# Optimization experiments

Measured on AMD Instinct MI355X. Metric: run time of the kernel, lower is better.

Reference implementation:

```python
import jax, jax.numpy as jnp
import numpy as np

M_CH = 3        # channel index from shapelet_info['pos'][1]
DIL = 4         # dilation
EPS = 1e-8      # pDic['scale_epsilon']


def setup_inputs() -> dict:
    key = jax.random.key(0)
    k1, k2 = jax.random.split(key, 2)
    B, C, Q, L = 512, 8, 4096, 32
    W = Q - (L - 1) * DIL  # 3972
    x = jax.random.normal(k1, (B, C, Q), dtype=jnp.float32)
    shapelet = jax.random.normal(k2, (L,), dtype=jnp.float32)
    posMap = jnp.zeros((W,), dtype=jnp.float32)
    posSlope = jnp.float32(1.0)
    return {"x": x, "shapelet": shapelet, "posMap": posMap, "posSlope": posSlope, "ep": 1}


def reference(x, shapelet, posMap, posSlope, ep):
    # x: [B, C, Q]; pick channel m, dilated unfold -> [B, W, L]
    B, C, Q = x.shape
    L = shapelet.shape[0]
    W = Q - (L - 1) * DIL
    xc = x[:, M_CH, :]                                        # [B, Q]
    idx = jnp.arange(W)[:, None] + jnp.arange(L)[None, :] * DIL  # [W, L]
    xu = xc[:, idx]                                           # [B, W, L]
    # scaleType == 2: z-normalize each subsequence (torch.std is unbiased -> ddof=1)
    mean = jnp.mean(xu, axis=-1, keepdims=True)
    std = jnp.std(xu, axis=-1, ddof=1, keepdims=True)
    xu = (xu - mean) / (std + EPS)
    # squared distance, mean over L
    d = jnp.mean((shapelet[None, None, :] - xu) ** 2, axis=-1)  # [B, W]
    # positional weighting: posSlope*elu(-posMap) + 2.0
    w = posSlope * jax.nn.elu(-posMap) + 2.0                  # [W]
    ftrs = d * w[None, :]                                     # [B, W] (sum over singleton channel dim is identity)
    agg = jnp.min(ftrs, axis=-1)                              # [B]
    return jax.nn.relu(agg)[:, None]                          # [B, 1]
```

## Files before the change

kernel.cpp:

```cpp
#include <hip/hip_runtime.h>
#include <math.h>

#define LC  32
#define QC  4096
#define WC  3972
#define NU  993
#define RUN 8

__device__ __forceinline__ int skew(int a) { return a + (a >> 6); }

__global__ __launch_bounds__(512, 4) void feature_kernel(
    const float* __restrict__ x,
    const float* __restrict__ shp,
    const float* __restrict__ posMap,
    const float* __restrict__ posSlope_p,
    float* __restrict__ out,
    int C)
{
    __shared__ float sx[4352];
    __shared__ float sw[4160];
    __shared__ float smin[8];

    const int tid   = threadIdx.x;
    const int b     = blockIdx.x;
    const float* __restrict__ xr = x + ((size_t)b * C + 3) * QC;

    {
        const float4* xr4 = reinterpret_cast<const float4*>(xr);
        #pragma unroll
        for (int i = 0; i < 2; ++i) {
            int a4 = tid + i * 512;
            float4 v = xr4[a4];
            int s = skew(a4 * 4);
            sx[s] = v.x; sx[s+1] = v.y; sx[s+2] = v.z; sx[s+3] = v.w;
        }
    }
    {
        const float ps = posSlope_p[0];
        const float4* pm4 = reinterpret_cast<const float4*>(posMap);
        #pragma unroll
        for (int i = 0; i < 2; ++i) {
            int a4 = tid + i * 512;
            if (a4 < NU) {
                float4 z = pm4[a4];
                float e0 = (-z.x > 0.f) ? -z.x : (__expf(-z.x) - 1.f);
                float e1 = (-z.y > 0.f) ? -z.y : (__expf(-z.y) - 1.f);
                float e2 = (-z.z > 0.f) ? -z.z : (__expf(-z.z) - 1.f);
                float e3 = (-z.w > 0.f) ? -z.w : (__expf(-z.w) - 1.f);
                int s = skew(a4 * 4);
                sw[s]   = fmaf(ps, e0, 2.0f);
                sw[s+1] = fmaf(ps, e1, 2.0f);
                sw[s+2] = fmaf(ps, e2, 2.0f);
                sw[s+3] = fmaf(ps, e3, 2.0f);
            }
        }
    }

    float sreg[LC];
    #pragma unroll
    for (int j = 0; j < LC; ++j) sreg[j] = shp[j];
    float Ssum = 0.f, S2 = 0.f;
    #pragma unroll
    for (int j = 0; j < LC; ++j) { Ssum += sreg[j]; S2 = fmaf(sreg[j], sreg[j], S2); }
    const float C0 = S2 * (1.0f / 32.0f) + 31.0f / 32.0f;

    __syncthreads();

    const int lane  = tid & 63;
    const int wv_id = tid >> 6;
    const int r     = wv_id & 3;
    const int gl    = ((wv_id >> 2) << 6) | lane;
    const int u0    = gl * RUN;
    const int w0    = r + 4 * u0;

    float buf[32];
    #pragma unroll
    for (int p = 0; p < 32; ++p)
        buf[p] = sx[skew(w0 + 4 * p)];

    float a0=0,a1=0,a2=0,a3=0, q0=0,q1=0,q2=0,q3=0;
    #pragma unroll
    for (int p = 0; p < 32; p += 4) {
        a0 += buf[p];   q0 = fmaf(buf[p],   buf[p],   q0);
        a1 += buf[p+1]; q1 = fmaf(buf[p+1], buf[p+1], q1);
        a2 += buf[p+2]; q2 = fmaf(buf[p+2], buf[p+2], q2);
        a3 += buf[p+3]; q3 = fmaf(buf[p+3], buf[p+3], q3);
    }
    float sum = (a0+a1)+(a2+a3);
    float sq  = (q0+q1)+(q2+q3);

    float best = INFINITY;

    #pragma unroll
    for (int k = 0; k < RUN; ++k) {
        if (k > 0) {
            int slot = (k + 31) & 31;
            float oldv = buf[slot];
            float newv = sx[skew(w0 + 4 * (k + 31))];
            sum += newv - oldv;
            sq  += fmaf(newv, newv, -(oldv * oldv));
            buf[slot] = newv;
        }
        float d0=0,d1=0,d2=0,d3=0;
        #pragma unroll
        for (int j = 0; j < LC; j += 4) {
            d0 = fmaf(sreg[j],   buf[(k+j)   & 31], d0);
            d1 = fmaf(sreg[j+1], buf[(k+j+1) & 31], d1);
            d2 = fmaf(sreg[j+2], buf[(k+j+2) & 31], d2);
            d3 = fmaf(sreg[j+3], buf[(k+j+3) & 31], d3);
        }
        float dot = (d0+d1)+(d2+d3);

        const int  u     = u0 + k;
        const bool valid = u < NU;
        float wvv = sw[skew(r + 4 * u)];

        float m   = sum * (1.0f / 32.0f);
        float var = (sq - 32.0f * m * m) * (1.0f / 31.0f);
        var = fmaxf(var, 1e-24f);
        float inv = __builtin_amdgcn_rsqf(var);
        float t   = fmaf(-m, Ssum, dot);
        float d   = fmaf(-t * (1.0f / 16.0f), inv, C0);
        float f   = valid ? d * wvv : INFINITY;
        best = fminf(best, f);
    }

    #pragma unroll
    for (int off = 32; off > 0; off >>= 1)
        best = fminf(best, __shfl_down(best, off, 64));
    if (lane == 0) smin[wv_id] = best;
    __syncthreads();
    if (tid == 0) {
        float m0 = fminf(fminf(smin[0], smin[1]), fminf(smin[2], smin[3]));
        float m1 = fminf(fminf(smin[4], smin[5]), fminf(smin[6], smin[7]));
        out[b] = fmaxf(fminf(m0, m1), 0.0f);
    }
}

extern "C" void kernel_launch(void* const* d_in, const int* in_sizes, int n_in,
                              void* d_out, int out_size, void* d_ws, size_t ws_size,
                              hipStream_t stream) {
    const float* x        = (const float*)d_in[0];
    const float* shp      = (const float*)d_in[1];
    const float* posMap   = (const float*)d_in[2];
    const float* posSlope = (const float*)d_in[3];
    float* out = (float*)d_out;

    const int C = 8;
    const int B = in_sizes[0] / (C * QC);

    feature_kernel<<<B, 512, 0, stream>>>(x, shp, posMap, posSlope, out, C);
}
```

Baseline: 11.31 us.

## Give each wavefront a private LDS slice to drop the block-wide barrier

Each of the 8 wavefronts now loads its own overlapping 640-element window of the channel row, plus its own slice of the position weights, into a private LDS region. It then replaces the __syncthreads before compute with a per-wave lgkmcnt wait. A new skew function (3 words of padding per 32) is meant to avoid LDS bank conflicts under the new lane-to-window mapping. This removes a block-wide barrier so waves can start computing independently. The cost is redundant global loads of the overlap regions (about 640 vs 512 elements per wave) and a larger LDS footprint, which could limit occupancy.

```diff
diff --git a/kernel.cpp b/kernel.cpp
--- a/kernel.cpp
+++ b/kernel.cpp
@@ -1,13 +1,13 @@
 #include <hip/hip_runtime.h>
 #include <math.h>
 
-#define LC  32
-#define QC  4096
-#define WC  3972
-#define NU  993
-#define RUN 8
-
-__device__ __forceinline__ int skew(int a) { return a + (a >> 6); }
+#define LC   32
+#define QC   4096
+#define WC   3972
+#define XSEG 640
+#define SKF(a) ((a) + 3 * ((a) >> 5))
+#define XPAD 700
+#define PPAD 560
 
 __global__ __launch_bounds__(512, 4) void feature_kernel(
     const float* __restrict__ x,
@@ -17,42 +17,57 @@
     float* __restrict__ out,
     int C)
 {
-    __shared__ float sx[4352];
-    __shared__ float sw[4160];
+    __shared__ float sx[8][XPAD];
+    __shared__ float sp[8][PPAD];
     __shared__ float smin[8];
 
-    const int tid   = threadIdx.x;
-    const int b     = blockIdx.x;
-    const float* __restrict__ xr = x + ((size_t)b * C + 3) * QC;
+    const int tid  = threadIdx.x;
+    const int b    = blockIdx.x;
+    const int lane = tid & 63;
+    const int v    = tid >> 6;
+    const int wb   = 496 * v;
+    const int Wlim = (v == 7) ? 500 : 496;
 
+    float* sxv = sx[v];
     {
-        const float4* xr4 = reinterpret_cast<const float4*>(xr);
+        const float4* xr4 = reinterpret_cast<const float4*>(
+            x + ((size_t)b * C + 3) * QC + wb);
         #pragma unroll
-        for (int i = 0; i < 2; ++i) {
-            int a4 = tid + i * 512;
-            float4 v = xr4[a4];
-            int s = skew(a4 * 4);
-            sx[s] = v.x; sx[s+1] = v.y; sx[s+2] = v.z; sx[s+3] = v.w;
+        for (int s = 0; s < 3; ++s) {
+            int i4 = lane + 64 * s;
+            if (i4 < XSEG / 4) {
+                float4 w4 = xr4[i4];
+                int sk = SKF(4 * i4);
+                sxv[sk] = w4.x; sxv[sk+1] = w4.y; sxv[sk+2] = w4.z; sxv[sk+3] = w4.w;
+            }
         }
     }
+    float* spv = sp[v];
     {
         const float ps = posSlope_p[0];
-        const float4* pm4 = reinterpret_cast<const float4*>(posMap);
         #pragma unroll
-        for (int i = 0; i < 2; ++i) {
-            int a4 = tid + i * 512;
-            if (a4 < NU) {
-                float4 z = pm4[a4];
-                float e0 = (-z.x > 0.f) ? -z.x : (__expf(-z.x) - 1.f);
-                float e1 = (-z.y > 0.f) ? -z.y : (__expf(-z.y) - 1.f);
-                float e2 = (-z.z > 0.f) ? -z.z : (__expf(-z.z) - 1.f);
-                float e3 = (-z.w > 0.f) ? -z.w : (__expf(-z.w) - 1.f);
-                int s = skew(a4 * 4);
-                sw[s]   = fmaf(ps, e0, 2.0f);
-                sw[s+1] = fmaf(ps, e1, 2.0f);
-                sw[s+2] = fmaf(ps, e2, 2.0f);
-                sw[s+3] = fmaf(ps, e3, 2.0f);
+        for (int s = 0; s < 2; ++s) {
+            int i4 = lane + 64 * s;
+            int g4 = 124 * v + i4;
+            float4 z;
+            if (g4 <= WC / 4 - 1) {
+                z = reinterpret_cast<const float4*>(posMap)[g4];
+            } else {
+                int g = 4 * g4;
+                z.x = posMap[min(g,     WC - 1)];
+                z.y = posMap[min(g + 1, WC - 1)];
+                z.z = posMap[min(g + 2, WC - 1)];
+                z.w = posMap[min(g + 3, WC - 1)];
             }
+            float e0 = (-z.x > 0.f) ? -z.x : (__expf(-z.x) - 1.f);
+            float e1 = (-z.y > 0.f) ? -z.y : (__expf(-z.y) - 1.f);
+            float e2 = (-z.z > 0.f) ? -z.z : (__expf(-z.z) - 1.f);
+            float e3 = (-z.w > 0.f) ? -z.w : (__expf(-z.w) - 1.f);
+            int sk = SKF(4 * i4);
+            spv[sk]   = fmaf(ps, e0, 2.0f);
+            spv[sk+1] = fmaf(ps, e1, 2.0f);
+            spv[sk+2] = fmaf(ps, e2, 2.0f);
+            spv[sk+3] = fmaf(ps, e3, 2.0f);
         }
     }
 
@@ -64,19 +79,16 @@
     for (int j = 0; j < LC; ++j) { Ssum += sreg[j]; S2 = fmaf(sreg[j], sreg[j], S2); }
     const float C0 = S2 * (1.0f / 32.0f) + 31.0f / 32.0f;
 
-    __syncthreads();
+    asm volatile("s_waitcnt lgkmcnt(0)" ::: "memory");
 
-    const int lane  = tid & 63;
-    const int wv_id = tid >> 6;
-    const int r     = wv_id & 3;
-    const int gl    = ((wv_id >> 2) << 6) | lane;
-    const int u0    = gl * RUN;
-    const int w0    = r + 4 * u0;
+    const int r   = lane & 3;
+    const int q   = lane >> 2;
+    const int w0l = r + 32 * q;
 
     float buf[32];
     #pragma unroll
     for (int p = 0; p < 32; ++p)
-        buf[p] = sx[skew(w0 + 4 * p)];
+        buf[p] = sxv[SKF(w0l + 4 * p)];
 
     float a0=0,a1=0,a2=0,a3=0, q0=0,q1=0,q2=0,q3=0;
     #pragma unroll
@@ -92,11 +104,11 @@
     float best = INFINITY;
 
     #pragma unroll
-    for (int k = 0; k < RUN; ++k) {
+    for (int k = 0; k < 8; ++k) {
         if (k > 0) {
             int slot = (k + 31) & 31;
             float oldv = buf[slot];
-            float newv = sx[skew(w0 + 4 * (k + 31))];
+            float newv = sxv[SKF(w0l + 4 * (k + 31))];
             sum += newv - oldv;
             sq  += fmaf(newv, newv, -(oldv * oldv));
             buf[slot] = newv;
@@ -111,9 +123,9 @@
         }
         float dot = (d0+d1)+(d2+d3);
 
-        const int  u     = u0 + k;
-        const bool valid = u < NU;
-        float wvv = sw[skew(r + 4 * u)];
+        const int  off   = w0l + 4 * k;
+        const bool valid = off < Wlim;
+        float wvv = spv[SKF(off)];
 
         float m   = sum * (1.0f / 32.0f);
         float var = (sq - 32.0f * m * m) * (1.0f / 31.0f);
@@ -128,7 +140,7 @@
     #pragma unroll
     for (int off = 32; off > 0; off >>= 1)
         best = fminf(best, __shfl_down(best, off, 64));
-    if (lane == 0) smin[wv_id] = best;
+    if (lane == 0) smin[v] = best;
     __syncthreads();
     if (tid == 0) {
         float m0 = fminf(fminf(smin[0], smin[1]), fminf(smin[2], smin[3]));
```

Result: slower. 12.34 us (+9.1%).
